# Optimization experiments

Hardware: AMD Instinct MI355X
Metric: run time of the kernel (lower is better)

Reference implementation:

```python
import jax, jax.numpy as jnp
import numpy as np
import math

B, N, W = 8, 2048, 512

def setup_inputs() -> dict:
    key0 = jax.random.key(0)
    ks = jax.random.split(key0, 6)
    return {
        "query": jax.random.normal(ks[0], (B, N, W), dtype=jnp.float32),
        "key":   jax.random.normal(ks[1], (B, N, W), dtype=jnp.float32),
        "W1": jax.random.normal(ks[2], (W, W), dtype=jnp.float32) * (1.0 / math.sqrt(W)),
        "b1": jax.random.normal(ks[3], (W,), dtype=jnp.float32) * 0.01,
        "W2": jax.random.normal(ks[4], (W, W), dtype=jnp.float32) * (1.0 / math.sqrt(W)),
        "b2": jax.random.normal(ks[5], (W,), dtype=jnp.float32) * 0.01,
    }

def _attn(q, k, v):
    # scores: [B, N, N]
    d_k = q.shape[-1]
    scores = jnp.einsum('bnd,bmd->bnm', q, k) / jnp.sqrt(jnp.asarray(d_k, q.dtype))
    p = jax.nn.softmax(scores, axis=-1)
    return jnp.einsum('bnm,bmd->bnd', p, v)

def reference(query, key, W1, b1, W2, b2):
    # nn.Linear: x @ W.T + b
    q = jnp.einsum('bnd,ed->bne', query, W1) + b1
    k = jnp.einsum('bnd,ed->bne', key, W2) + b2
    x1 = _attn(q, k, q)  # attention(query, key, query)
    x2 = _attn(k, q, k)  # attention(key, query, key)
    return jnp.concatenate((x1, x2), axis=1)  # [B, 2N, W]
```

## Files before the change

kernel.cpp:

```cpp
#include <hip/hip_runtime.h>
#include <hip/hip_bf16.h>
#include <stdint.h>

typedef unsigned short ushort_t;
typedef __attribute__((ext_vector_type(8))) short short8;
typedef __attribute__((ext_vector_type(4))) short short4v;
typedef __attribute__((ext_vector_type(4))) float f32x4;

__device__ inline ushort_t f2bf(float x) {
  uint32_t u = __float_as_uint(x);
  u += 0x7fffu + ((u >> 16) & 1u);
  return (ushort_t)(u >> 16);
}
__device__ inline float bfu2f(uint32_t h) { return __uint_as_float(h << 16); }

__device__ inline uint32_t pk2bf(float a, float b) {
  __hip_bfloat162 h = __float22bfloat162_rn(make_float2(a, b));
  union { __hip_bfloat162 h2; uint32_t u; } cv; cv.h2 = h; return cv.u;
}

__device__ inline void gload_lds16(const void* g, void* l) {
  __builtin_amdgcn_global_load_lds((const __attribute__((address_space(1))) uint32_t*)g,
                                   (__attribute__((address_space(3))) uint32_t*)l, 16, 0, 0);
}

__global__ __launch_bounds__(512, 2) void linear_kernel(
    const float* __restrict__ query, const float* __restrict__ key,
    const float* __restrict__ W1, const float* __restrict__ b1,
    const float* __restrict__ W2, const float* __restrict__ b2,
    ushort_t* __restrict__ q_bf, ushort_t* __restrict__ k_bf,
    ushort_t* __restrict__ qT, ushort_t* __restrict__ kT)
{
  extern __shared__ __attribute__((aligned(16))) ushort_t smL[];

  int bx = blockIdx.x;
  int which = bx & 1, rt = bx >> 1;
  const float* X    = which ? key : query;
  const float* Wm   = which ? W2  : W1;
  const float* bias = which ? b2  : b1;
  ushort_t* OUT  = which ? k_bf : q_bf;
  ushort_t* OUTT = which ? kT   : qT;

  int t = threadIdx.x, w = t >> 6, lane = t & 63, g = lane >> 4, m = lane & 15;

  {
    int tp = t & 127, rsub = t >> 7;
#pragma unroll 4
    for (int p = 0; p < 32; ++p) {
      int row = p * 4 + rsub;
      f32x4 v = *(const f32x4*)(X + (size_t)(rt * 128 + row) * 512 + tp * 4);
      uint2 dv;
      dv.x = pk2bf(v[0], v[1]);
      dv.y = pk2bf(v[2], v[3]);
      int chunk = tp >> 1;
      int phys = chunk ^ (row & 7);
      *(uint2*)&smL[row * 512 + phys * 8 + (tp & 1) * 4] = dv;
    }
  }
  __syncthreads();

  f32x4 zero = {0.f, 0.f, 0.f, 0.f};
  f32x4 acc[8][4];
#pragma unroll
  for (int i = 0; i < 8; ++i)
#pragma unroll
    for (int j = 0; j < 4; ++j) acc[i][j] = zero;

  const float* Wbase = Wm + (size_t)(w * 64) * 512;

  for (int k0 = 0; k0 < 16; ++k0) {
    short8 bfr[4];
#pragma unroll
    for (int j = 0; j < 4; ++j) {
      const float* wp = Wbase + (size_t)(16 * j + m) * 512 + k0 * 32 + g * 8;
      f32x4 lo = *(const f32x4*)wp;
      f32x4 hi = *(const f32x4*)(wp + 4);
      union { uint32_t u[4]; short8 s; } fb;
      fb.u[0] = pk2bf(lo[0], lo[1]); fb.u[1] = pk2bf(lo[2], lo[3]);
      fb.u[2] = pk2bf(hi[0], hi[1]); fb.u[3] = pk2bf(hi[2], hi[3]);
      bfr[j] = fb.s;
    }
    short8 afr[8];
#pragma unroll
    for (int i = 0; i < 8; ++i) {
      int row = 16 * i + m;
      int phys = (k0 * 4 + g) ^ (m & 7);
      afr[i] = *(const short8*)&smL[row * 512 + phys * 8];
    }
#pragma unroll
    for (int i = 0; i < 8; ++i)
#pragma unroll
      for (int j = 0; j < 4; ++j)
        acc[i][j] = __builtin_amdgcn_mfma_f32_16x16x32_bf16(afr[i], bfr[j], acc[i][j], 0, 0, 0);
  }

  float bw[4];
#pragma unroll
  for (int j = 0; j < 4; ++j) bw[j] = bias[w * 64 + 16 * j + m];

  __syncthreads();

#pragma unroll
  for (int j = 0; j < 4; ++j)
#pragma unroll
    for (int i = 0; i < 8; ++i) {
      f32x4 c4 = acc[i][j];
#pragma unroll
      for (int rr = 0; rr < 4; ++rr)
        smL[(16 * i + 4 * g + rr) * 520 + w * 64 + 16 * j + m] = f2bf(c4[rr] + bw[j]);
    }
  __syncthreads();
  {
    int row = t >> 2, qtr = t & 3;
    size_t gb = (size_t)(rt * 128 + row) * 512 + qtr * 128;
#pragma unroll
    for (int i2 = 0; i2 < 16; ++i2)
      *(short8*)(OUT + gb + i2 * 8) = *(const short8*)&smL[row * 520 + qtr * 128 + i2 * 8];
  }
  __syncthreads();

#pragma unroll
  for (int j = 0; j < 4; ++j)
#pragma unroll
    for (int i = 0; i < 8; ++i) {
      f32x4 c4 = acc[i][j];
      short4v tv;
#pragma unroll
      for (int rr = 0; rr < 4; ++rr) tv[rr] = (short)f2bf(c4[rr] + bw[j]);
      *(short4v*)&smL[(w * 64 + 16 * j + m) * 136 + 16 * i + 4 * g] = tv;
    }
  __syncthreads();
  {
    size_t b_ = (size_t)(rt >> 4);
    size_t gb = b_ * (512 * 2048) + (size_t)t * 2048 + (size_t)(rt & 15) * 128;
#pragma unroll
    for (int i2 = 0; i2 < 16; ++i2)
      *(short8*)(OUTT + gb + i2 * 8) = *(const short8*)&smL[t * 136 + i2 * 8];
  }
}

__global__ __launch_bounds__(512, 2) void attn_kernel(
    const ushort_t* __restrict__ qb, const ushort_t* __restrict__ kb_,
    const ushort_t* __restrict__ qT, const ushort_t* __restrict__ kT,
    float* __restrict__ out)
{
  extern __shared__ ushort_t sm[];
  const float CEXP = 1.4426950408889634f / 22.62741699796952f;

  int bx = blockIdx.x;
  int group = bx & 15, mtile = bx >> 4;
  int b = group >> 1, att = group & 1;
  const ushort_t* Qp = (att ? kb_ : qb) + (size_t)b * (2048 * 512);
  const ushort_t* Kp = (att ? qb  : kb_) + (size_t)b * (2048 * 512);
  const ushort_t* Vt = (att ? kT  : qT)  + (size_t)b * (512 * 2048);

  int t = threadIdx.x, w = t >> 6, lane = t & 63, g = lane >> 4, m = lane & 15;
  int wq = w >> 1, dh = w & 1;
  int qrow = mtile * 128 + w * 16 + m;
  int sw8  = ((g ^ ((m >> 1) & 3)) * 8);
  int srow = lane >> 2;
  int soff = ((lane & 3) ^ ((lane >> 3) & 3)) * 8;
  int pm6 = (m & 6);

  ushort_t* Plds = sm + 65536;
  float* lbuf = (float*)(sm + 69632);

  int pw0 = (w * 16 + m) * 32 + ((g ^ pm6) << 2);
  int pw1 = (w * 16 + m) * 32 + (((g + 4) ^ pm6) << 2);
  int pr0 = (wq * 32 +      m) * 32 + (((2 * g) ^ pm6) << 2);
  int pr1 = (wq * 32 + 16 + m) * 32 + (((2 * g) ^ pm6) << 2);

  short8 qf[16];
#pragma unroll
  for (int ks = 0; ks < 16; ++ks)
    qf[ks] = *(const short8*)(Qp + (size_t)qrow * 512 + ks * 32 + g * 8);

  f32x4 zero = {0.f, 0.f, 0.f, 0.f};
  f32x4 acc[16][2];
#pragma unroll
  for (int dt = 0; dt < 16; ++dt) { acc[dt][0] = zero; acc[dt][1] = zero; }
  float l = 0.f;

  auto stage = [&](int buf, int kb) {
    ushort_t* base = sm + buf * 32768;
    const int kbase = kb * 32;
#pragma unroll
    for (int i = 0; i < 4; ++i) {
      int qi = w * 4 + i, ks = qi >> 1, tt2 = qi & 1;
      const ushort_t* gsrc = Kp + (size_t)(kbase + tt2 * 16 + srow) * 512 + ks * 32 + soff;
      gload_lds16(gsrc, base + ks * 1024 + tt2 * 512);
    }
#pragma unroll
    for (int i = 0; i < 4; ++i) {
      int qi = w * 4 + i;
      const ushort_t* gsrc = Vt + (size_t)(qi * 16 + srow) * 2048 + kbase + soff;
      gload_lds16(gsrc, base + 16384 + qi * 512);
    }
  };

  stage(0, 0);

  for (int kb = 0; kb < 64; ++kb) {
    int cur = kb & 1;
    __syncthreads();
    if (kb + 1 < 64) stage(1 - cur, kb + 1);
    const ushort_t* base = sm + cur * 32768;

    f32x4 T0 = zero, T1 = zero;
    __builtin_amdgcn_s_setprio(1);
#pragma unroll
    for (int ks = 0; ks < 16; ++ks) {
      short8 k0 = *(const short8*)&base[ks * 1024 +       m * 32 + sw8];
      short8 k1 = *(const short8*)&base[ks * 1024 + 512 + m * 32 + sw8];
      T0 = __builtin_amdgcn_mfma_f32_16x16x32_bf16(k0, qf[ks], T0, 0, 0, 0);
      T1 = __builtin_amdgcn_mfma_f32_16x16x32_bf16(k1, qf[ks], T1, 0, 0, 0);
    }
    __builtin_amdgcn_s_setprio(0);

    uint32_t h[8];
#pragma unroll
    for (int r = 0; r < 4; ++r) {
      float e0 = __builtin_amdgcn_exp2f(T0[r] * CEXP);
      float e1 = __builtin_amdgcn_exp2f(T1[r] * CEXP);
      h[r]     = f2bf(e0);
      h[4 + r] = f2bf(e1);
      l += bfu2f(h[r]) + bfu2f(h[4 + r]);
    }
    uint2 p0, p1;
    p0.x = h[0] | (h[1] << 16); p0.y = h[2] | (h[3] << 16);
    p1.x = h[4] | (h[5] << 16); p1.y = h[6] | (h[7] << 16);
    *(uint2*)&Plds[pw0] = p0;
    *(uint2*)&Plds[pw1] = p1;

    __syncthreads();

    short8 pf0 = *(const short8*)&Plds[pr0];
    short8 pf1 = *(const short8*)&Plds[pr1];
    __builtin_amdgcn_s_setprio(1);
#pragma unroll
    for (int dt = 0; dt < 16; ++dt) {
      short8 vf = *(const short8*)&base[16384 + (dh * 16 + dt) * 512 + m * 32 + sw8];
      acc[dt][0] = __builtin_amdgcn_mfma_f32_16x16x32_bf16(vf, pf0, acc[dt][0], 0, 0, 0);
      acc[dt][1] = __builtin_amdgcn_mfma_f32_16x16x32_bf16(vf, pf1, acc[dt][1], 0, 0, 0);
    }
    __builtin_amdgcn_s_setprio(0);
  }

  l += __shfl_xor(l, 16, 64);
  l += __shfl_xor(l, 32, 64);
  if (lane < 16) lbuf[w * 16 + lane] = 1.0f / l;
  __syncthreads();

  float inv0 = lbuf[wq * 32 + m];
  float inv1 = lbuf[wq * 32 + 16 + m];
  size_t orow0 = (size_t)b * 4096 + (size_t)att * 2048 + mtile * 128 + wq * 32 + m;
  float* ob0 = out + orow0 * 512 + dh * 256;
  float* ob1 = out + (orow0 + 16) * 512 + dh * 256;
#pragma unroll
  for (int dt = 0; dt < 16; ++dt) {
    f32x4 v0 = acc[dt][0] * inv0;
    *(f32x4*)(ob0 + dt * 16 + g * 4) = v0;
  }
#pragma unroll
  for (int dt = 0; dt < 16; ++dt) {
    f32x4 v1 = acc[dt][1] * inv1;
    *(f32x4*)(ob1 + dt * 16 + g * 4) = v1;
  }
}

extern "C" void kernel_launch(void* const* d_in, const int* in_sizes, int n_in,
                              void* d_out, int out_size, void* d_ws, size_t ws_size,
                              hipStream_t stream) {
  const float* query = (const float*)d_in[0];
  const float* key   = (const float*)d_in[1];
  const float* W1    = (const float*)d_in[2];
  const float* b1    = (const float*)d_in[3];
  const float* W2    = (const float*)d_in[4];
  const float* b2    = (const float*)d_in[5];
  float* out = (float*)d_out;

  ushort_t* ws   = (ushort_t*)d_ws;
  ushort_t* q_bf = ws;
  ushort_t* k_bf = ws + 8388608;
  ushort_t* qT   = ws + 16777216;
  ushort_t* kT   = ws + 25165824;

  (void)hipFuncSetAttribute((const void*)linear_kernel,
                            hipFuncAttributeMaxDynamicSharedMemorySize, 139264);
  (void)hipFuncSetAttribute((const void*)attn_kernel,
                            hipFuncAttributeMaxDynamicSharedMemorySize, 139776);

  linear_kernel<<<256, 512, 139264, stream>>>(query, key, W1, b1, W2, b2,
                                              q_bf, k_bf, qT, kT);
  attn_kernel<<<256, 512, 139776, stream>>>(q_bf, k_bf, qT, kT, out);
}
```

Measured before the change: 320.9 us.

## Halve linear row tile and regroup attention PV warps for more reuse

```diff
diff --git a/kernel.cpp b/kernel.cpp
--- a/kernel.cpp
+++ b/kernel.cpp
@@ -24,7 +24,7 @@
                                    (__attribute__((address_space(3))) uint32_t*)l, 16, 0, 0);
 }
 
-__global__ __launch_bounds__(512, 2) void linear_kernel(
+__global__ __launch_bounds__(512, 4) void linear_kernel(
     const float* __restrict__ query, const float* __restrict__ key,
     const float* __restrict__ W1, const float* __restrict__ b1,
     const float* __restrict__ W2, const float* __restrict__ b2,
@@ -46,9 +46,9 @@
   {
     int tp = t & 127, rsub = t >> 7;
 #pragma unroll 4
-    for (int p = 0; p < 32; ++p) {
+    for (int p = 0; p < 16; ++p) {
       int row = p * 4 + rsub;
-      f32x4 v = *(const f32x4*)(X + (size_t)(rt * 128 + row) * 512 + tp * 4);
+      f32x4 v = *(const f32x4*)(X + (size_t)(rt * 64 + row) * 512 + tp * 4);
       uint2 dv;
       dv.x = pk2bf(v[0], v[1]);
       dv.y = pk2bf(v[2], v[3]);
@@ -60,9 +60,9 @@
   __syncthreads();
 
   f32x4 zero = {0.f, 0.f, 0.f, 0.f};
-  f32x4 acc[8][4];
-#pragma unroll
-  for (int i = 0; i < 8; ++i)
+  f32x4 acc[4][4];
+#pragma unroll
+  for (int i = 0; i < 4; ++i)
 #pragma unroll
     for (int j = 0; j < 4; ++j) acc[i][j] = zero;
 
@@ -80,15 +80,15 @@
       fb.u[2] = pk2bf(hi[0], hi[1]); fb.u[3] = pk2bf(hi[2], hi[3]);
       bfr[j] = fb.s;
     }
-    short8 afr[8];
-#pragma unroll
-    for (int i = 0; i < 8; ++i) {
+    short8 afr[4];
+#pragma unroll
+    for (int i = 0; i < 4; ++i) {
       int row = 16 * i + m;
       int phys = (k0 * 4 + g) ^ (m & 7);
       afr[i] = *(const short8*)&smL[row * 512 + phys * 8];
     }
 #pragma unroll
-    for (int i = 0; i < 8; ++i)
+    for (int i = 0; i < 4; ++i)
 #pragma unroll
       for (int j = 0; j < 4; ++j)
         acc[i][j] = __builtin_amdgcn_mfma_f32_16x16x32_bf16(afr[i], bfr[j], acc[i][j], 0, 0, 0);
@@ -103,7 +103,7 @@
 #pragma unroll
   for (int j = 0; j < 4; ++j)
 #pragma unroll
-    for (int i = 0; i < 8; ++i) {
+    for (int i = 0; i < 4; ++i) {
       f32x4 c4 = acc[i][j];
 #pragma unroll
       for (int rr = 0; rr < 4; ++rr)
@@ -111,31 +111,31 @@
     }
   __syncthreads();
   {
-    int row = t >> 2, qtr = t & 3;
-    size_t gb = (size_t)(rt * 128 + row) * 512 + qtr * 128;
-#pragma unroll
-    for (int i2 = 0; i2 < 16; ++i2)
-      *(short8*)(OUT + gb + i2 * 8) = *(const short8*)&smL[row * 520 + qtr * 128 + i2 * 8];
+    int row = t >> 3, oct = t & 7;
+    size_t gb = (size_t)(rt * 64 + row) * 512 + oct * 64;
+#pragma unroll
+    for (int i2 = 0; i2 < 8; ++i2)
+      *(short8*)(OUT + gb + i2 * 8) = *(const short8*)&smL[row * 520 + oct * 64 + i2 * 8];
   }
   __syncthreads();
 
 #pragma unroll
   for (int j = 0; j < 4; ++j)
 #pragma unroll
-    for (int i = 0; i < 8; ++i) {
+    for (int i = 0; i < 4; ++i) {
       f32x4 c4 = acc[i][j];
       short4v tv;
 #pragma unroll
       for (int rr = 0; rr < 4; ++rr) tv[rr] = (short)f2bf(c4[rr] + bw[j]);
-      *(short4v*)&smL[(w * 64 + 16 * j + m) * 136 + 16 * i + 4 * g] = tv;
+      *(short4v*)&smL[(w * 64 + 16 * j + m) * 68 + 16 * i + 4 * g] = tv;
     }
   __syncthreads();
   {
-    size_t b_ = (size_t)(rt >> 4);
-    size_t gb = b_ * (512 * 2048) + (size_t)t * 2048 + (size_t)(rt & 15) * 128;
-#pragma unroll
-    for (int i2 = 0; i2 < 16; ++i2)
-      *(short8*)(OUTT + gb + i2 * 8) = *(const short8*)&smL[t * 136 + i2 * 8];
+    size_t b_ = (size_t)(rt >> 5);
+    size_t gb = b_ * (512 * 2048) + (size_t)t * 2048 + (size_t)(rt & 31) * 64;
+#pragma unroll
+    for (int i2 = 0; i2 < 8; ++i2)
+      *(short8*)(OUTT + gb + i2 * 8) = *(const short8*)&smL[t * 68 + i2 * 8];
   }
 }
 
@@ -155,7 +155,7 @@
   const ushort_t* Vt = (att ? kT  : qT)  + (size_t)b * (512 * 2048);
 
   int t = threadIdx.x, w = t >> 6, lane = t & 63, g = lane >> 4, m = lane & 15;
-  int wq = w >> 1, dh = w & 1;
+  int dq = w >> 1, qh = w & 1;
   int qrow = mtile * 128 + w * 16 + m;
   int sw8  = ((g ^ ((m >> 1) & 3)) * 8);
   int srow = lane >> 2;
@@ -167,8 +167,10 @@
 
   int pw0 = (w * 16 + m) * 32 + ((g ^ pm6) << 2);
   int pw1 = (w * 16 + m) * 32 + (((g + 4) ^ pm6) << 2);
-  int pr0 = (wq * 32 +      m) * 32 + (((2 * g) ^ pm6) << 2);
-  int pr1 = (wq * 32 + 16 + m) * 32 + (((2 * g) ^ pm6) << 2);
+  int prq[4];
+#pragma unroll
+  for (int qt = 0; qt < 4; ++qt)
+    prq[qt] = (qh * 64 + qt * 16 + m) * 32 + (((2 * g) ^ pm6) << 2);
 
   short8 qf[16];
 #pragma unroll
@@ -176,9 +178,11 @@
     qf[ks] = *(const short8*)(Qp + (size_t)qrow * 512 + ks * 32 + g * 8);
 
   f32x4 zero = {0.f, 0.f, 0.f, 0.f};
-  f32x4 acc[16][2];
-#pragma unroll
-  for (int dt = 0; dt < 16; ++dt) { acc[dt][0] = zero; acc[dt][1] = zero; }
+  f32x4 acc[8][4];
+#pragma unroll
+  for (int dt = 0; dt < 8; ++dt)
+#pragma unroll
+    for (int qt = 0; qt < 4; ++qt) acc[dt][qt] = zero;
   float l = 0.f;
 
   auto stage = [&](int buf, int kb) {
@@ -234,14 +238,16 @@
 
     __syncthreads();
 
-    short8 pf0 = *(const short8*)&Plds[pr0];
-    short8 pf1 = *(const short8*)&Plds[pr1];
+    short8 pf[4];
+#pragma unroll
+    for (int qt = 0; qt < 4; ++qt) pf[qt] = *(const short8*)&Plds[prq[qt]];
     __builtin_amdgcn_s_setprio(1);
 #pragma unroll
-    for (int dt = 0; dt < 16; ++dt) {
-      short8 vf = *(const short8*)&base[16384 + (dh * 16 + dt) * 512 + m * 32 + sw8];
-      acc[dt][0] = __builtin_amdgcn_mfma_f32_16x16x32_bf16(vf, pf0, acc[dt][0], 0, 0, 0);
-      acc[dt][1] = __builtin_amdgcn_mfma_f32_16x16x32_bf16(vf, pf1, acc[dt][1], 0, 0, 0);
+    for (int dt = 0; dt < 8; ++dt) {
+      short8 vf = *(const short8*)&base[16384 + (dq * 8 + dt) * 512 + m * 32 + sw8];
+#pragma unroll
+      for (int qt = 0; qt < 4; ++qt)
+        acc[dt][qt] = __builtin_amdgcn_mfma_f32_16x16x32_bf16(vf, pf[qt], acc[dt][qt], 0, 0, 0);
     }
     __builtin_amdgcn_s_setprio(0);
   }
@@ -251,20 +257,18 @@
   if (lane < 16) lbuf[w * 16 + lane] = 1.0f / l;
   __syncthreads();
 
-  float inv0 = lbuf[wq * 32 + m];
-  float inv1 = lbuf[wq * 32 + 16 + m];
-  size_t orow0 = (size_t)b * 4096 + (size_t)att * 2048 + mtile * 128 + wq * 32 + m;
-  float* ob0 = out + orow0 * 512 + dh * 256;
-  float* ob1 = out + (orow0 + 16) * 512 + dh * 256;
-#pragma unroll
-  for (int dt = 0; dt < 16; ++dt) {
-    f32x4 v0 = acc[dt][0] * inv0;
-    *(f32x4*)(ob0 + dt * 16 + g * 4) = v0;
-  }
-#pragma unroll
-  for (int dt = 0; dt < 16; ++dt) {
-    f32x4 v1 = acc[dt][1] * inv1;
-    *(f32x4*)(ob1 + dt * 16 + g * 4) = v1;
+  float inv[4];
+#pragma unroll
+  for (int qt = 0; qt < 4; ++qt) inv[qt] = lbuf[qh * 64 + qt * 16 + m];
+  size_t orow = (size_t)b * 4096 + (size_t)att * 2048 + mtile * 128 + qh * 64 + m;
+#pragma unroll
+  for (int qt = 0; qt < 4; ++qt) {
+    float* ob = out + (orow + qt * 16) * 512 + dq * 128;
+#pragma unroll
+    for (int dt = 0; dt < 8; ++dt) {
+      f32x4 v = acc[dt][qt] * inv[qt];
+      *(f32x4*)(ob + dt * 16 + g * 4) = v;
+    }
   }
 }
 
@@ -286,11 +290,11 @@
   ushort_t* kT   = ws + 25165824;
 
   (void)hipFuncSetAttribute((const void*)linear_kernel,
-                            hipFuncAttributeMaxDynamicSharedMemorySize, 139264);
+                            hipFuncAttributeMaxDynamicSharedMemorySize, 69632);
   (void)hipFuncSetAttribute((const void*)attn_kernel,
                             hipFuncAttributeMaxDynamicSharedMemorySize, 139776);
 
-  linear_kernel<<<256, 512, 139264, stream>>>(query, key, W1, b1, W2, b2,
-                                              q_bf, k_bf, qT, kT);
+  linear_kernel<<<512, 512, 69632, stream>>>(query, key, W1, b1, W2, b2,
+                                             q_bf, k_bf, qT, kT);
   attn_kernel<<<256, 512, 139776, stream>>>(q_bf, k_bf, qT, kT, out);
 }
```

New measurement: 331.9 us. 1.03x slower.
